# Optimization experiments

Hardware: AMD Instinct MI355X
Metric: run time of the kernel (lower is better)

The kernel has to match this reference:

```python
import jax, jax.numpy as jnp
import numpy as np

# ModernBERT-base, local (sliding-window) attention layer (layer_id=1, global every 3)
B, S, H = 2, 4096, 768
NH, HD = 12, 64          # num heads, head dim
WINDOW = 128             # config.local_attention -> +/- WINDOW//2 tokens
ROPE_THETA = 10000.0     # local rope theta
NEG = jnp.float32(-1e9)


def setup_inputs() -> dict:
    key = jax.random.key(0)
    k1, k2, k3 = jax.random.split(key, 3)
    hidden_states = jax.random.normal(k1, (B, S, H), dtype=jnp.float32)
    Wqkv = jax.random.normal(k2, (3 * H, H), dtype=jnp.float32) * 0.02
    Wo = jax.random.normal(k3, (H, H), dtype=jnp.float32) * 0.02
    position_ids = jnp.broadcast_to(jnp.arange(S, dtype=jnp.int32), (B, S))
    # additive masks, [1,1,S,S] broadcast over batch/heads
    attention_mask = jnp.zeros((1, 1, S, S), dtype=jnp.float32)  # full attention (all visible)
    idx = jnp.arange(S)
    dist = jnp.abs(idx[:, None] - idx[None, :])
    sliding_window_mask = jnp.where(dist <= WINDOW // 2, 0.0, NEG).astype(jnp.float32)[None, None]
    return {
        "hidden_states": hidden_states,
        "attention_mask": attention_mask,
        "sliding_window_mask": sliding_window_mask,
        "position_ids": position_ids,
        "Wqkv": Wqkv,
        "Wo": Wo,
    }


def _rope_cos_sin(position_ids):
    inv_freq = 1.0 / (ROPE_THETA ** (jnp.arange(0, HD, 2, dtype=jnp.float32) / HD))  # [HD/2]
    freqs = position_ids.astype(jnp.float32)[..., None] * inv_freq  # [B,S,HD/2]
    emb = jnp.concatenate([freqs, freqs], axis=-1)  # [B,S,HD]
    return jnp.cos(emb), jnp.sin(emb)


def _rotate_half(x):
    x1, x2 = jnp.split(x, 2, axis=-1)
    return jnp.concatenate([-x2, x1], axis=-1)


def reference(hidden_states, attention_mask, sliding_window_mask, position_ids, Wqkv, Wo):
    qkv = jnp.einsum('bsh,oh->bso', hidden_states, Wqkv)  # [B,S,3H]
    q, k, v = jnp.split(qkv, 3, axis=-1)
    q = q.reshape(B, S, NH, HD)
    k = k.reshape(B, S, NH, HD)
    v = v.reshape(B, S, NH, HD)
    cos, sin = _rope_cos_sin(position_ids)  # [B,S,HD]
    cos, sin = cos[:, :, None, :], sin[:, :, None, :]
    q = q * cos + _rotate_half(q) * sin
    k = k * cos + _rotate_half(k) * sin
    # layer_id=1 -> sliding window (local) layer
    mask = sliding_window_mask
    scale = 1.0 / jnp.sqrt(jnp.float32(HD))
    scores = jnp.einsum('bqnd,bknd->bnqk', q, k) * scale + mask  # [B,NH,S,S]
    probs = jax.nn.softmax(scores, axis=-1)
    attn = jnp.einsum('bnqk,bknd->bqnd', probs, v).reshape(B, S, H)
    out = jnp.einsum('bsh,oh->bso', attn, Wo)  # dropout p=0 (eval)
    return out
```

## Files before the change

### kernel.cpp

```cpp
#include <hip/hip_runtime.h>
#include <hip/hip_bf16.h>
#include <math.h>

#define BB 2
#define SS 4096
#define HH 768
#define NHEADS 12
#define MTOT (BB*SS)
#define NQKV (3*HH)

typedef _Float16 f16;
typedef __attribute__((ext_vector_type(8))) _Float16 f16x8;
typedef __attribute__((ext_vector_type(4))) _Float16 f16x4;
typedef __attribute__((ext_vector_type(4))) float f32x4;

__device__ __forceinline__ void gld_lds16(const void* g, void* l) {
  __builtin_amdgcn_global_load_lds(
      (const __attribute__((address_space(1))) unsigned int*)g,
      (__attribute__((address_space(3))) unsigned int*)l, 16, 0, 0);
}

__global__ __launch_bounds__(256)
void cvt_kernel(const float* __restrict__ src, f16* __restrict__ dst, int n4) {
  int i = blockIdx.x * 256 + threadIdx.x;
  if (i >= n4) return;
  float4 v = reinterpret_cast<const float4*>(src)[i];
  f16x4 o;
  o[0] = (f16)v.x; o[1] = (f16)v.y; o[2] = (f16)v.z; o[3] = (f16)v.w;
  reinterpret_cast<f16x4*>(dst)[i] = o;
}

__global__ void rope_table_kernel(float* __restrict__ ctab, float* __restrict__ stab) {
  int idx = blockIdx.x * 256 + threadIdx.x;
  if (idx >= SS * 32) return;
  int s = idx >> 5;
  int j = idx & 31;
  const double r = 0.7498942093324559;
  double inv = 1.0;
  for (int t = 0; t < j; ++t) inv *= r;
  double ph = (double)s * inv;
  const double TWO_PI = 6.283185307179586;
  double red = ph - TWO_PI * floor(ph / TWO_PI);
  float rf = (float)red;
  ctab[idx] = cosf(rf);
  stab[idx] = sinf(rf);
}

template<int EPI>
__global__ __launch_bounds__(256)
void gemm_f16(const f16* __restrict__ A, const f16* __restrict__ Bw,
              float* __restrict__ C,
              f16* __restrict__ Oq, f16* __restrict__ Ok, f16* __restrict__ Ov,
              const int* __restrict__ pos,
              const float* __restrict__ ctab, const float* __restrict__ stab,
              int Mtiles, int N, int K) {
  __shared__ __align__(16) f16 As[3][128][32];
  __shared__ __align__(16) f16 Bs[3][128][32];
  const int tid = threadIdx.x;
  const int lane = tid & 63;
  const int w = tid >> 6;
  const int wr = w >> 1, wc = w & 1;

  const int bid = blockIdx.x;
  const int xcd = bid & 7;
  const int idx = bid >> 3;
  const int mch = Mtiles >> 3;
  const int bm = (xcd * mch + (idx % mch)) * 128;
  const int bn = (idx / mch) * 128;

  f32x4 acc[4][4] = {};

  const int l4 = lane >> 2;
  const int lk = lane & 3;
  const int srow = w * 32;
  const int fr = lane & 15;
  const int fst = (l4 >> 1) & 3;
  const int pc = (((lane >> 4) ^ ((fr >> 1) & 3)) * 8);

  auto stage = [&](int buf, int k0) {
#pragma unroll
    for (int i = 0; i < 2; ++i) {
      int row = srow + i * 16 + l4;
      gld_lds16(A + (size_t)(bm + row) * K + k0 + (lk ^ fst) * 8,
                (char*)&As[0][0][0] + buf * 8192 + w * 2048 + i * 1024 + lane * 16);
      gld_lds16(Bw + (size_t)(bn + row) * K + k0 + (lk ^ fst) * 8,
                (char*)&Bs[0][0][0] + buf * 8192 + w * 2048 + i * 1024 + lane * 16);
    }
  };
  auto compute = [&](int buf) {
    f16x8 av[4], bv[4];
#pragma unroll
    for (int m = 0; m < 4; ++m)
      av[m] = *reinterpret_cast<const f16x8*>(&As[buf][wr * 64 + m * 16 + fr][pc]);
#pragma unroll
    for (int n = 0; n < 4; ++n)
      bv[n] = *reinterpret_cast<const f16x8*>(&Bs[buf][wc * 64 + n * 16 + fr][pc]);
    __builtin_amdgcn_s_setprio(1);
#pragma unroll
    for (int m = 0; m < 4; ++m)
#pragma unroll
      for (int n = 0; n < 4; ++n)
        acc[m][n] = __builtin_amdgcn_mfma_f32_16x16x32_f16(av[m], bv[n],
                                                           acc[m][n], 0, 0, 0);
    __builtin_amdgcn_s_setprio(0);
  };

  const int T = K >> 5;
  stage(0, 0);
  stage(1, 32);
  for (int t = 0; t < T; ++t) {
    if (t == T - 1)
      asm volatile("s_waitcnt vmcnt(0)" ::: "memory");
    else
      asm volatile("s_waitcnt vmcnt(4)" ::: "memory");
    __builtin_amdgcn_s_barrier();
    __builtin_amdgcn_sched_barrier(0);
    if (t + 2 < T) stage((t + 2) % 3, (t + 2) << 5);
    compute(t % 3);
  }

  const int cl = lane & 15;
  const int rg = lane >> 4;
  if (EPI == 0) {
#pragma unroll
    for (int m = 0; m < 4; ++m)
#pragma unroll
      for (int n = 0; n < 4; ++n)
#pragma unroll
        for (int r = 0; r < 4; ++r) {
          int row = bm + wr * 64 + m * 16 + rg * 4 + r;
          int col = bn + wc * 64 + n * 16 + cl;
          C[(size_t)row * N + col] = acc[m][n][r];
        }
  } else {
    const int sec = bn / HH;
    f16* dst = (sec == 0) ? Oq : ((sec == 1) ? Ok : Ov);
    const int hb = bn - sec * HH + wc * 64;
#pragma unroll
    for (int m = 0; m < 4; ++m)
#pragma unroll
      for (int r = 0; r < 4; ++r) {
        int row = bm + wr * 64 + m * 16 + rg * 4 + r;
        if (sec < 2) {
          int s = pos[row];
#pragma unroll
          for (int n = 0; n < 4; ++n) {
            int hd = hb + n * 16 + cl;
            int d = hd & 63;
            int d2 = d & 31;
            float c = ctab[s * 32 + d2];
            float sn = stab[s * 32 + d2];
            float val = acc[m][n][r];
            float pv = acc[m][n ^ 2][r];
            val = (d < 32) ? (val * c - pv * sn) : (val * c + pv * sn);
            if (sec == 0) val *= 0.125f;
            dst[(size_t)row * HH + hd] = (f16)val;
          }
        } else {
#pragma unroll
          for (int n = 0; n < 4; ++n)
            dst[(size_t)row * HH + hb + n * 16 + cl] = (f16)acc[m][n][r];
        }
      }
  }
}

#define AQT 64
#define AKT 192
#define KP 72
#define VP 200

__global__ __launch_bounds__(256)
void attn_kernel(const f16* __restrict__ qg, const f16* __restrict__ kg,
                 const f16* __restrict__ vg, f16* __restrict__ og) {
  __shared__ __align__(16) f16 Qs[AQT][KP];
  __shared__ __align__(16) f16 Ks[AKT][KP];
  __shared__ __align__(16) f16 Vs[64][VP];
  __shared__ float sums[AQT];

  const int tid = threadIdx.x;
  const int lane = tid & 63;
  const int wq = tid >> 6;
  const int l15 = lane & 15, g = lane >> 4;
  const int blk = blockIdx.x;
  const int qt = blk % (SS / AQT);
  const int h = (blk / (SS / AQT)) % NHEADS;
  const int b = blk / ((SS / AQT) * NHEADS);
  const int q0 = qt * AQT;
  const int kbase = q0 - 64;

#pragma unroll
  for (int i = 0; i < 2; ++i) {
    int idx = tid + i * 256;
    int r = idx >> 3, ch = idx & 7;
    f16x8 v = *reinterpret_cast<const f16x8*>(
        &qg[((size_t)(b * SS + q0 + r)) * HH + h * 64 + ch * 8]);
    *reinterpret_cast<f16x8*>(&Qs[r][ch * 8]) = v;
  }
#pragma unroll
  for (int i = 0; i < 6; ++i) {
    int idx = tid + i * 256;
    int r = idx >> 3, ch = idx & 7;
    int kglob = kbase + r;
    f16x8 v = {};
    if (kglob >= 0 && kglob < SS)
      v = *reinterpret_cast<const f16x8*>(
          &kg[((size_t)(b * SS + kglob)) * HH + h * 64 + ch * 8]);
    *reinterpret_cast<f16x8*>(&Ks[r][ch * 8]) = v;
  }
#pragma unroll
  for (int i = 0; i < 6; ++i) {
    int idx = tid + i * 256;
    int r = idx >> 3, ch = idx & 7;
    int kglob = kbase + r;
    f16x8 v = {};
    if (kglob >= 0 && kglob < SS)
      v = *reinterpret_cast<const f16x8*>(
          &vg[((size_t)(b * SS + kglob)) * HH + h * 64 + ch * 8]);
#pragma unroll
    for (int j = 0; j < 8; ++j) Vs[ch * 8 + j][r] = v[j];
  }
  __syncthreads();

  f32x4 accs[12] = {};
#pragma unroll
  for (int kd = 0; kd < 2; ++kd) {
    f16x8 bq = *reinterpret_cast<const f16x8*>(&Qs[wq * 16 + l15][kd * 32 + g * 8]);
#pragma unroll
    for (int f = 0; f < 12; ++f) {
      f16x8 ak = *reinterpret_cast<const f16x8*>(&Ks[f * 16 + l15][kd * 32 + g * 8]);
      accs[f] = __builtin_amdgcn_mfma_f32_16x16x32_f16(ak, bq, accs[f], 0, 0, 0);
    }
  }
  __syncthreads();

  const int qloc = wq * 16 + l15;
  float mx = -1e30f;
#pragma unroll
  for (int f = 0; f < 12; ++f)
#pragma unroll
    for (int r = 0; r < 4; ++r) {
      int key = f * 16 + g * 4 + r;
      int kglob = kbase + key;
      bool valid = (key >= qloc) && (key <= qloc + 128) && (kglob >= 0) && (kglob < SS);
      float s = valid ? accs[f][r] : -1e30f;
      accs[f][r] = s;
      mx = fmaxf(mx, s);
    }
  mx = fmaxf(mx, __shfl_xor(mx, 16));
  mx = fmaxf(mx, __shfl_xor(mx, 32));
  f16* Ps = &Ks[0][0];
  float sum = 0.f;
#pragma unroll
  for (int f = 0; f < 12; ++f) {
    float p0 = __expf(accs[f][0] - mx);
    float p1 = __expf(accs[f][1] - mx);
    float p2 = __expf(accs[f][2] - mx);
    float p3 = __expf(accs[f][3] - mx);
    sum += (p0 + p1) + (p2 + p3);
    f16x4 pk;
    pk[0] = (f16)p0; pk[1] = (f16)p1; pk[2] = (f16)p2; pk[3] = (f16)p3;
    *reinterpret_cast<f16x4*>(&Ps[(size_t)qloc * VP + f * 16 + g * 4]) = pk;
  }
  sum += __shfl_xor(sum, 16);
  sum += __shfl_xor(sum, 32);
  if (g == 0) sums[qloc] = sum;

  f32x4 acco[4] = {};
#pragma unroll
  for (int ks = 0; ks < 6; ++ks) {
    f16x8 pa = *reinterpret_cast<const f16x8*>(&Ps[(size_t)(wq * 16 + l15) * VP + ks * 32 + g * 8]);
#pragma unroll
    for (int n = 0; n < 4; ++n) {
      f16x8 bv = *reinterpret_cast<const f16x8*>(&Vs[n * 16 + l15][ks * 32 + g * 8]);
      acco[n] = __builtin_amdgcn_mfma_f32_16x16x32_f16(pa, bv, acco[n], 0, 0, 0);
    }
  }
#pragma unroll
  for (int r = 0; r < 4; ++r) {
    int qo = wq * 16 + g * 4 + r;
    float inv = 1.0f / sums[qo];
    size_t base = ((size_t)(b * SS + q0 + qo)) * HH + h * 64;
#pragma unroll
    for (int n = 0; n < 4; ++n)
      og[base + n * 16 + l15] = (f16)(acco[n][r] * inv);
  }
}

extern "C" void kernel_launch(void* const* d_in, const int* in_sizes, int n_in,
                              void* d_out, int out_size, void* d_ws, size_t ws_size,
                              hipStream_t stream) {
  const float* hs = (const float*)d_in[0];
  const int* pos = (const int*)d_in[3];
  const float* Wqkv = (const float*)d_in[4];
  const float* Wo = (const float*)d_in[5];
  float* out = (float*)d_out;

  uint8_t* ws = (uint8_t*)d_ws;
  size_t off = 0;
  float* ctab = (float*)(ws + off); off += (size_t)SS * 32 * 4;
  float* stab = (float*)(ws + off); off += (size_t)SS * 32 * 4;
  f16* hs16 = (f16*)(ws + off); off += (size_t)MTOT * HH * 2;
  f16* wq16 = (f16*)(ws + off); off += (size_t)NQKV * HH * 2;
  f16* wo16 = (f16*)(ws + off); off += (size_t)HH * HH * 2;
  f16* qf = (f16*)(ws + off); off += (size_t)MTOT * HH * 2;
  f16* kf = (f16*)(ws + off); off += (size_t)MTOT * HH * 2;
  f16* vf = (f16*)(ws + off); off += (size_t)MTOT * HH * 2;
  f16* af = (f16*)(ws + off); off += (size_t)MTOT * HH * 2;

  cvt_kernel<<<(MTOT * HH / 4 + 255) / 256, 256, 0, stream>>>(hs, hs16, MTOT * HH / 4);
  cvt_kernel<<<(NQKV * HH / 4 + 255) / 256, 256, 0, stream>>>(Wqkv, wq16, NQKV * HH / 4);
  cvt_kernel<<<(HH * HH / 4 + 255) / 256, 256, 0, stream>>>(Wo, wo16, HH * HH / 4);
  rope_table_kernel<<<(SS * 32 + 255) / 256, 256, 0, stream>>>(ctab, stab);

  gemm_f16<1><<<(MTOT / 128) * (NQKV / 128), 256, 0, stream>>>(
      hs16, wq16, nullptr, qf, kf, vf, pos, ctab, stab, MTOT / 128, NQKV, HH);
  attn_kernel<<<BB * NHEADS * (SS / AQT), 256, 0, stream>>>(qf, kf, vf, af);
  gemm_f16<0><<<(MTOT / 128) * (HH / 128), 256, 0, stream>>>(
      af, wo16, out, nullptr, nullptr, nullptr, nullptr, nullptr, nullptr,
      MTOT / 128, HH, HH);
}
```

Before: 121.2 us.

## Use 256x256-tile, 512-thread QKV GEMM with swizzled LDS and phased prefetch

Replaces the templated 128x128 QKV projection GEMM with a dedicated kernel using 256x256 output tiles, 8 waves, K-steps of 64, double-buffered LDS with an XOR swizzle, and loads for the next K-step interleaved between four compute phases. It also raises wave priority around the MFMA bursts. The larger tile raises arithmetic intensity and cuts redundant global loads of A and B. The cost is 288 blocks on a 256-CU part, which gives uneven wave quantization, plus heavy register use for 32 accumulators per lane. The output GEMM becomes a plain non-templated kernel.

```diff
diff --git a/kernel.cpp b/kernel.cpp
--- a/kernel.cpp
+++ b/kernel.cpp
@@ -46,14 +46,136 @@
   stab[idx] = sinf(rf);
 }
 
-template<int EPI>
+__global__ __launch_bounds__(512)
+void gemm1_256(const f16* __restrict__ A, const f16* __restrict__ Bw,
+               f16* __restrict__ Oq, f16* __restrict__ Ok, f16* __restrict__ Ov,
+               const int* __restrict__ pos,
+               const float* __restrict__ ctab, const float* __restrict__ stab) {
+  __shared__ __align__(16) f16 As[2][256][64];
+  __shared__ __align__(16) f16 Bs[2][256][64];
+  const int K = HH;
+  const int tid = threadIdx.x;
+  const int lane = tid & 63;
+  const int w = tid >> 6;
+  const int wr = w >> 2, wc = w & 3;
+
+  const int bid = blockIdx.x;
+  const int xcd = bid & 7;
+  const int idx = bid >> 3;
+  const int bm = (xcd * 4 + (idx & 3)) * 256;
+  const int bn = (idx >> 2) * 256;
+
+  f32x4 acc[8][4] = {};
+
+  const int trow = tid >> 3;
+  const int gsw = (tid & 7) ^ (trow & 7);
+  const int fr = lane & 15;
+  const int g16 = lane >> 4;
+
+  auto stage = [&](int slot, int ph, int k0) {
+    const f16* src = (ph < 2) ? A : Bw;
+    const int hh = ph & 1;
+    const int rbase = ((ph < 2) ? bm : bn) + hh * 128;
+    char* dstbase = ((ph < 2) ? (char*)&As[slot][0][0] : (char*)&Bs[slot][0][0])
+                    + hh * 16384;
+#pragma unroll
+    for (int i = 0; i < 2; ++i)
+      gld_lds16(src + (size_t)(rbase + i * 64 + trow) * K + k0 + gsw * 8,
+                dstbase + i * 8192 + tid * 16);
+  };
+
+  auto phase = [&](int slot, int q) {
+    const int mh = q >> 1, nh = q & 1;
+    f16x8 av[4][2], bv[2][2];
+#pragma unroll
+    for (int m2 = 0; m2 < 4; ++m2) {
+      const int R = wr * 128 + (mh * 4 + m2) * 16 + fr;
+#pragma unroll
+      for (int kk = 0; kk < 2; ++kk)
+        av[m2][kk] = *reinterpret_cast<const f16x8*>(
+            &As[slot][R][((kk * 4 + g16) ^ (R & 7)) * 8]);
+    }
+#pragma unroll
+    for (int n2 = 0; n2 < 2; ++n2) {
+      const int R = wc * 64 + (nh * 2 + n2) * 16 + fr;
+#pragma unroll
+      for (int kk = 0; kk < 2; ++kk)
+        bv[n2][kk] = *reinterpret_cast<const f16x8*>(
+            &Bs[slot][R][((kk * 4 + g16) ^ (R & 7)) * 8]);
+    }
+    asm volatile("s_waitcnt lgkmcnt(0)" ::: "memory");
+    __builtin_amdgcn_sched_barrier(0);
+    __builtin_amdgcn_s_setprio(1);
+#pragma unroll
+    for (int kk = 0; kk < 2; ++kk)
+#pragma unroll
+      for (int m2 = 0; m2 < 4; ++m2)
+#pragma unroll
+        for (int n2 = 0; n2 < 2; ++n2)
+          acc[mh * 4 + m2][nh * 2 + n2] = __builtin_amdgcn_mfma_f32_16x16x32_f16(
+              av[m2][kk], bv[n2][kk], acc[mh * 4 + m2][nh * 2 + n2], 0, 0, 0);
+    __builtin_amdgcn_s_setprio(0);
+  };
+
+  const int T = 12;
+  stage(0, 0, 0); stage(0, 1, 0); stage(0, 2, 0); stage(0, 3, 0);
+  for (int t = 0; t < T; ++t) {
+    const int s = t & 1;
+    const int k1 = (t + 1) << 6;
+    if (t + 1 < T) {
+      stage(s ^ 1, 0, k1);
+      asm volatile("s_waitcnt vmcnt(2)" ::: "memory");
+    } else {
+      asm volatile("s_waitcnt vmcnt(0)" ::: "memory");
+    }
+    __builtin_amdgcn_s_barrier();
+    __builtin_amdgcn_sched_barrier(0);
+    phase(s, 0);
+    if (t + 1 < T) stage(s ^ 1, 1, k1);
+    phase(s, 1);
+    if (t + 1 < T) stage(s ^ 1, 2, k1);
+    phase(s, 2);
+    if (t + 1 < T) stage(s ^ 1, 3, k1);
+    phase(s, 3);
+    __builtin_amdgcn_s_barrier();
+  }
+
+  const int cl = lane & 15;
+  const int rg = lane >> 4;
+  const int sec = bn / HH;
+  f16* dst = (sec == 0) ? Oq : ((sec == 1) ? Ok : Ov);
+  const int hb = bn - sec * HH + wc * 64;
+#pragma unroll
+  for (int m = 0; m < 8; ++m)
+#pragma unroll
+    for (int r = 0; r < 4; ++r) {
+      const int row = bm + wr * 128 + m * 16 + rg * 4 + r;
+      if (sec < 2) {
+        const int sp = pos[row];
+#pragma unroll
+        for (int n = 0; n < 4; ++n) {
+          const int hd = hb + n * 16 + cl;
+          const int d = hd & 63;
+          const int d2 = d & 31;
+          const float c = ctab[sp * 32 + d2];
+          const float sn = stab[sp * 32 + d2];
+          float val = acc[m][n][r];
+          const float pv = acc[m][n ^ 2][r];
+          val = (d < 32) ? (val * c - pv * sn) : (val * c + pv * sn);
+          if (sec == 0) val *= 0.125f;
+          dst[(size_t)row * HH + hd] = (f16)val;
+        }
+      } else {
+#pragma unroll
+        for (int n = 0; n < 4; ++n)
+          dst[(size_t)row * HH + hb + n * 16 + cl] = (f16)acc[m][n][r];
+      }
+    }
+}
+
 __global__ __launch_bounds__(256)
-void gemm_f16(const f16* __restrict__ A, const f16* __restrict__ Bw,
-              float* __restrict__ C,
-              f16* __restrict__ Oq, f16* __restrict__ Ok, f16* __restrict__ Ov,
-              const int* __restrict__ pos,
-              const float* __restrict__ ctab, const float* __restrict__ stab,
-              int Mtiles, int N, int K) {
+void gemm2_f16(const f16* __restrict__ A, const f16* __restrict__ Bw,
+               float* __restrict__ C, int Mtiles, int N, int K) {
   __shared__ __align__(16) f16 As[3][128][32];
   __shared__ __align__(16) f16 Bs[3][128][32];
   const int tid = threadIdx.x;
@@ -121,48 +243,16 @@
 
   const int cl = lane & 15;
   const int rg = lane >> 4;
-  if (EPI == 0) {
-#pragma unroll
-    for (int m = 0; m < 4; ++m)
-#pragma unroll
-      for (int n = 0; n < 4; ++n)
-#pragma unroll
-        for (int r = 0; r < 4; ++r) {
-          int row = bm + wr * 64 + m * 16 + rg * 4 + r;
-          int col = bn + wc * 64 + n * 16 + cl;
-          C[(size_t)row * N + col] = acc[m][n][r];
-        }
-  } else {
-    const int sec = bn / HH;
-    f16* dst = (sec == 0) ? Oq : ((sec == 1) ? Ok : Ov);
-    const int hb = bn - sec * HH + wc * 64;
-#pragma unroll
-    for (int m = 0; m < 4; ++m)
+#pragma unroll
+  for (int m = 0; m < 4; ++m)
+#pragma unroll
+    for (int n = 0; n < 4; ++n)
 #pragma unroll
       for (int r = 0; r < 4; ++r) {
         int row = bm + wr * 64 + m * 16 + rg * 4 + r;
-        if (sec < 2) {
-          int s = pos[row];
-#pragma unroll
-          for (int n = 0; n < 4; ++n) {
-            int hd = hb + n * 16 + cl;
-            int d = hd & 63;
-            int d2 = d & 31;
-            float c = ctab[s * 32 + d2];
-            float sn = stab[s * 32 + d2];
-            float val = acc[m][n][r];
-            float pv = acc[m][n ^ 2][r];
-            val = (d < 32) ? (val * c - pv * sn) : (val * c + pv * sn);
-            if (sec == 0) val *= 0.125f;
-            dst[(size_t)row * HH + hd] = (f16)val;
-          }
-        } else {
-#pragma unroll
-          for (int n = 0; n < 4; ++n)
-            dst[(size_t)row * HH + hb + n * 16 + cl] = (f16)acc[m][n][r];
-        }
+        int col = bn + wc * 64 + n * 16 + cl;
+        C[(size_t)row * N + col] = acc[m][n][r];
       }
-  }
 }
 
 #define AQT 64
@@ -313,10 +403,9 @@
   cvt_kernel<<<(HH * HH / 4 + 255) / 256, 256, 0, stream>>>(Wo, wo16, HH * HH / 4);
   rope_table_kernel<<<(SS * 32 + 255) / 256, 256, 0, stream>>>(ctab, stab);
 
-  gemm_f16<1><<<(MTOT / 128) * (NQKV / 128), 256, 0, stream>>>(
-      hs16, wq16, nullptr, qf, kf, vf, pos, ctab, stab, MTOT / 128, NQKV, HH);
+  gemm1_256<<<(MTOT / 256) * (NQKV / 256), 512, 0, stream>>>(
+      hs16, wq16, qf, kf, vf, pos, ctab, stab);
   attn_kernel<<<BB * NHEADS * (SS / AQT), 256, 0, stream>>>(qf, kf, vf, af);
-  gemm_f16<0><<<(MTOT / 128) * (HH / 128), 256, 0, stream>>>(
-      af, wo16, out, nullptr, nullptr, nullptr, nullptr, nullptr, nullptr,
-      MTOT / 128, HH, HH);
-}
+  gemm2_f16<<<(MTOT / 128) * (HH / 128), 256, 0, stream>>>(
+      af, wo16, out, MTOT / 128, HH, HH);
+}
```

New measurement: 133.7 us. 10.3% more time.
